# Optimization experiments

Hardware: AMD Instinct MI355X
Metric: run time of the kernel (lower is better)

Reference implementation:

```python
import jax, jax.numpy as jnp
import numpy as np

FRAME, LATENT, HIDDEN, GATE_H, EXPERTS = 267, 32, 256, 64, 6
BATCH = 4096
IN0 = LATENT + FRAME            # 299: decoder layer-0 input (z, c)
IN1 = LATENT + HIDDEN           # 288: decoder layer-1/2 input (z, h)
OUT = FRAME                     # num_future_predictions * frame_size


def _lin(key, fan_in, fan_out):
    b = np.sqrt(1.0 / fan_in)
    return jax.random.uniform(key, (fan_in, fan_out), jnp.float32, -b, b)


def setup_inputs() -> dict:
    key = jax.random.key(0)
    ks = jax.random.split(key, 16)
    d = {
        "x": jax.random.normal(ks[0], (BATCH, FRAME), jnp.float32),
        "c": jax.random.normal(ks[1], (BATCH, FRAME), jnp.float32),
        "eps": jax.random.normal(ks[2], (BATCH, LATENT), jnp.float32),
        # encoder
        "enc_w1": _lin(ks[3], 2 * FRAME, HIDDEN), "enc_b1": jnp.zeros((HIDDEN,), jnp.float32),
        "enc_w2": _lin(ks[4], FRAME + HIDDEN, HIDDEN), "enc_b2": jnp.zeros((HIDDEN,), jnp.float32),
        "enc_wmu": _lin(ks[5], FRAME + HIDDEN, LATENT), "enc_bmu": jnp.zeros((LATENT,), jnp.float32),
        "enc_wlv": _lin(ks[6], FRAME + HIDDEN, LATENT), "enc_blv": jnp.zeros((LATENT,), jnp.float32),
        # gate MLP
        "g_w0": _lin(ks[7], IN0, GATE_H), "g_b0": jnp.zeros((GATE_H,), jnp.float32),
        "g_w1": _lin(ks[8], GATE_H, GATE_H), "g_b1": jnp.zeros((GATE_H,), jnp.float32),
        "g_w2": _lin(ks[9], GATE_H, EXPERTS), "g_b2": jnp.zeros((EXPERTS,), jnp.float32),
        # expert-mixed decoder layers (kaiming-uniform-ish init, bias 0.01)
        "w0": jax.random.uniform(ks[10], (EXPERTS, IN0, HIDDEN), jnp.float32, -np.sqrt(6.0 / IN0), np.sqrt(6.0 / IN0)),
        "b0": jnp.full((EXPERTS, HIDDEN), 0.01, jnp.float32),
        "w1": jax.random.uniform(ks[11], (EXPERTS, IN1, HIDDEN), jnp.float32, -np.sqrt(6.0 / IN1), np.sqrt(6.0 / IN1)),
        "b1": jnp.full((EXPERTS, HIDDEN), 0.01, jnp.float32),
        "w2": jax.random.uniform(ks[12], (EXPERTS, IN1, OUT), jnp.float32, -np.sqrt(6.0 / IN1), np.sqrt(6.0 / IN1)),
        "b2": jnp.full((EXPERTS, OUT), 0.01, jnp.float32),
    }
    return d


def reference(x, c, eps,
              enc_w1, enc_b1, enc_w2, enc_b2, enc_wmu, enc_bmu, enc_wlv, enc_blv,
              g_w0, g_b0, g_w1, g_b1, g_w2, g_b2,
              w0, b0, w1, b1, w2, b2):
    elu = jax.nn.elu
    # --- encoder ---
    h1 = elu(jnp.concatenate([x, c], axis=1) @ enc_w1 + enc_b1)
    h2 = elu(jnp.concatenate([x, h1], axis=1) @ enc_w2 + enc_b2)
    s = jnp.concatenate([x, h2], axis=1)
    mu = s @ enc_wmu + enc_bmu
    logvar = s @ enc_wlv + enc_blv
    z = mu + eps * jnp.exp(0.5 * logvar)
    # --- gate ---
    zc = jnp.concatenate([z, c], axis=1)
    g = elu(zc @ g_w0 + g_b0)
    g = elu(g @ g_w1 + g_b1)
    coeff = jax.nn.softmax(g @ g_w2 + g_b2, axis=1)  # [N, E]
    # --- soft-MoE decoder: blended-weight per-sample GEMMs ---
    layer = c
    for w, b, act in ((w0, b0, elu), (w1, b1, elu), (w2, b2, None)):
        inp = jnp.concatenate([z, layer], axis=1)  # [N, Din]
        # out[n,o] = sum_e coeff[n,e] * (inp[n,:] @ w[e,:,o]) + coeff[n,:] @ b[:,o]
        out = jnp.einsum('ne,ni,eio->no', coeff, inp, w) + coeff @ b
        layer = act(out) if act is not None else out
    return layer, mu, logvar
```

## Files before the change

### kernel.cpp

```cpp
#include <hip/hip_runtime.h>
#include <hip/hip_bf16.h>
#include <math.h>

#define N_BATCH 4096
#define FRAME   267
#define LATENT  32
#define HIDDEN  256
#define GATE_H  64
#define EXPERTS 6

typedef __hip_bfloat16 bf16;
typedef __bf16  bf16x8 __attribute__((ext_vector_type(8)));
typedef float   f32x4  __attribute__((ext_vector_type(4)));

__device__ __forceinline__ float eluf(float v) { return (v > 0.f) ? v : (expf(v) - 1.f); }

#define MFMA(a, b, p) __builtin_amdgcn_mfma_f32_16x16x32_bf16((a), (b), (p), 0, 0, 0)

struct WEnt { const float* src; bf16* dst; int K, M, Mtot, mOff, Ksteps, Mtiles, cum; };
struct WTab { WEnt e[10]; int total; };

__global__ __launch_bounds__(256) void prep_kernel(
    const float* __restrict__ bmu, const float* __restrict__ blv,
    float* __restrict__ biasCat, WTab tab)
{
    const int tid = threadIdx.x, bid = blockIdx.x;
    if (bid == 0 && tid < 64)
        biasCat[tid] = (tid < 32) ? bmu[tid] : blv[tid - 32];

    __shared__ float tbuf[32][33];
    int i = 0;
    while (i < 9 && bid >= tab.e[i + 1].cum) ++i;
    const WEnt en = tab.e[i];
    const int t = bid - en.cum;
    const int perE = en.Ksteps * en.Mtiles;
    const int e = t / perE;
    const int rr = t - e * perE;
    const int mt = rr / en.Ksteps;
    const int ks = rr - mt * en.Ksteps;
    const int tx = tid & 31, ty = tid >> 5;
    const float* src = en.src + (size_t)e * en.K * en.M;
    #pragma unroll
    for (int i0 = 0; i0 < 32; i0 += 8) {
        const int k = ks * 32 + i0 + ty, m = mt * 32 + tx;
        tbuf[i0 + ty][tx] = (k < en.K && m < en.M) ? src[(size_t)k * en.M + m] : 0.f;
    }
    __syncthreads();
    bf16* dst = en.dst + ((size_t)(e * en.Ksteps + ks) * en.Mtot + en.mOff + mt * 32) * 32;
    #pragma unroll
    for (int i0 = 0; i0 < 32; i0 += 8)
        dst[(size_t)(i0 + ty) * 32 + tx] = __float2bfloat16(tbuf[tx][i0 + ty]);
}

__global__ __launch_bounds__(512, 2) void fused_kernel(
    const float* __restrict__ x, const float* __restrict__ c,
    const float* __restrict__ eps,
    const bf16* __restrict__ We1, const float* __restrict__ eb1,
    const bf16* __restrict__ We2, const float* __restrict__ eb2,
    const bf16* __restrict__ Wml, const float* __restrict__ biasCat,
    const bf16* __restrict__ Wg0, const float* __restrict__ gb0,
    const bf16* __restrict__ Wg1, const float* __restrict__ gb1,
    const bf16* __restrict__ Wg2, const float* __restrict__ gb2,
    const bf16* __restrict__ W0, const float* __restrict__ b0,
    const bf16* __restrict__ W1, const float* __restrict__ b1,
    const bf16* __restrict__ W2, const float* __restrict__ b2,
    float* __restrict__ out_layer, float* __restrict__ out_mu,
    float* __restrict__ out_lv)
{
    __shared__ bf16  bufA[16 * 552];
    __shared__ bf16  bufB[16 * 552];
    __shared__ float sML[16 * 64];
    __shared__ bf16  sG1[16 * 72];
    __shared__ bf16  sG2[16 * 72];
    __shared__ float sLg[16 * 16];
    __shared__ float sCo[EXPERTS * 16];

    const int tid  = threadIdx.x;
    const int w    = tid >> 6, lane = tid & 63, ml = lane & 15, quad = lane >> 4;
    const int row0 = blockIdx.x * 16;
    const int r32  = tid >> 5, l32 = tid & 31;

    {
        const float* xr = x + (size_t)(row0 + r32) * FRAME;
        const float* cr = c + (size_t)(row0 + r32) * FRAME;
        #pragma unroll
        for (int j = 0; j < 17; ++j) {
            const int col = l32 + j * 32;
            float v = 0.f;
            if (col < FRAME)          v = xr[col];
            else if (col < 2 * FRAME) v = cr[col - FRAME];
            bufA[r32 * 552 + col] = __float2bfloat16(v);
        }
    }
    __syncthreads();

    {
        bf16x8 av[17];
        #pragma unroll
        for (int ks = 0; ks < 17; ++ks)
            av[ks] = *(const bf16x8*)(bufA + ml * 552 + ks * 32 + quad * 8);
        const int col0 = 32 * w + ml;
        f32x4 p0 = (f32x4){0,0,0,0}, p1 = (f32x4){0,0,0,0};
        const bf16* wp = We1 + (size_t)col0 * 32 + quad * 8;
        #pragma unroll
        for (int ks = 0; ks < 17; ++ks) {
            p0 = MFMA(av[ks], *(const bf16x8*)(wp + (size_t)ks * 256 * 32), p0);
            p1 = MFMA(av[ks], *(const bf16x8*)(wp + (size_t)ks * 256 * 32 + 16 * 32), p1);
        }
        const float bv0 = eb1[col0], bv1 = eb1[col0 + 16];
        #pragma unroll
        for (int rg = 0; rg < 4; ++rg) {
            bufB[(quad * 4 + rg) * 552 + 267 + col0]      = __float2bfloat16(eluf(p0[rg] + bv0));
            bufB[(quad * 4 + rg) * 552 + 267 + col0 + 16] = __float2bfloat16(eluf(p1[rg] + bv1));
        }
        #pragma unroll
        for (int j = 0; j < 9; ++j) {
            const int cc = l32 + j * 32;
            if (cc < 267) bufB[r32 * 552 + cc] = bufA[r32 * 552 + cc];
            else          bufB[r32 * 552 + (cc - 267 + 523)] = __float2bfloat16(0.f);
        }
    }
    __syncthreads();

    {
        bf16x8 av[17];
        #pragma unroll
        for (int ks = 0; ks < 17; ++ks)
            av[ks] = *(const bf16x8*)(bufB + ml * 552 + ks * 32 + quad * 8);
        const int col0 = 32 * w + ml;
        f32x4 p0 = (f32x4){0,0,0,0}, p1 = (f32x4){0,0,0,0};
        const bf16* wp = We2 + (size_t)col0 * 32 + quad * 8;
        #pragma unroll
        for (int ks = 0; ks < 17; ++ks) {
            p0 = MFMA(av[ks], *(const bf16x8*)(wp + (size_t)ks * 256 * 32), p0);
            p1 = MFMA(av[ks], *(const bf16x8*)(wp + (size_t)ks * 256 * 32 + 16 * 32), p1);
        }
        __syncthreads();
        const float bv0 = eb2[col0], bv1 = eb2[col0 + 16];
        #pragma unroll
        for (int rg = 0; rg < 4; ++rg) {
            bufB[(quad * 4 + rg) * 552 + 267 + col0]      = __float2bfloat16(eluf(p0[rg] + bv0));
            bufB[(quad * 4 + rg) * 552 + 267 + col0 + 16] = __float2bfloat16(eluf(p1[rg] + bv1));
        }
    }
    __syncthreads();

    if (w < 4) {
        const int col = 16 * w + ml;
        f32x4 p = (f32x4){0,0,0,0};
        const bf16* wp = Wml + (size_t)col * 32 + quad * 8;
        #pragma unroll
        for (int ks = 0; ks < 17; ++ks) {
            const bf16x8 av = *(const bf16x8*)(bufB + ml * 552 + ks * 32 + quad * 8);
            p = MFMA(av, *(const bf16x8*)(wp + (size_t)ks * 64 * 32), p);
        }
        const float bv = biasCat[col];
        #pragma unroll
        for (int rg = 0; rg < 4; ++rg)
            sML[(quad * 4 + rg) * 64 + col] = p[rg] + bv;
    }
    __syncthreads();

    {
        const float m  = sML[r32 * 64 + l32];
        const float lv = sML[r32 * 64 + 32 + l32];
        const int gi = (row0 + r32) * LATENT + l32;
        out_mu[gi] = m; out_lv[gi] = lv;
        const bf16 zb = __float2bfloat16(m + eps[gi] * expf(0.5f * lv));
        bufA[r32 * 552 + l32] = zb;
        bufB[r32 * 552 + l32] = zb;
        #pragma unroll
        for (int j = 0; j < 9; ++j) {
            const int col = 32 + l32 + j * 32;
            bf16 v = __float2bfloat16(0.f);
            if (col < 299) v = bufA[r32 * 552 + 267 + (col - 32)];
            bufB[r32 * 552 + col] = v;
        }
    }
    __syncthreads();

    if (w < 4) {
        const int col = 16 * w + ml;
        f32x4 p = (f32x4){0,0,0,0};
        const bf16* wp = Wg0 + (size_t)col * 32 + quad * 8;
        #pragma unroll
        for (int ks = 0; ks < 10; ++ks)
            p = MFMA(*(const bf16x8*)(bufB + ml * 552 + ks * 32 + quad * 8),
                     *(const bf16x8*)(wp + (size_t)ks * 64 * 32), p);
        const float bv = gb0[col];
        #pragma unroll
        for (int rg = 0; rg < 4; ++rg)
            sG1[(quad * 4 + rg) * 72 + col] = __float2bfloat16(eluf(p[rg] + bv));
    }
    __syncthreads();

    if (w < 4) {
        const int col = 16 * w + ml;
        f32x4 p = (f32x4){0,0,0,0};
        const bf16* wp = Wg1 + (size_t)col * 32 + quad * 8;
        #pragma unroll
        for (int ks = 0; ks < 2; ++ks)
            p = MFMA(*(const bf16x8*)(sG1 + ml * 72 + ks * 32 + quad * 8),
                     *(const bf16x8*)(wp + (size_t)ks * 64 * 32), p);
        const float bv = gb1[col];
        #pragma unroll
        for (int rg = 0; rg < 4; ++rg)
            sG2[(quad * 4 + rg) * 72 + col] = __float2bfloat16(eluf(p[rg] + bv));
    }
    __syncthreads();

    if (w == 0) {
        f32x4 p = (f32x4){0,0,0,0};
        const bf16* wp = Wg2 + (size_t)ml * 32 + quad * 8;
        #pragma unroll
        for (int ks = 0; ks < 2; ++ks)
            p = MFMA(*(const bf16x8*)(sG2 + ml * 72 + ks * 32 + quad * 8),
                     *(const bf16x8*)(wp + (size_t)ks * 32 * 32), p);
        const float bv = (ml < EXPERTS) ? gb2[ml] : 0.f;
        #pragma unroll
        for (int rg = 0; rg < 4; ++rg)
            sLg[(quad * 4 + rg) * 16 + ml] = p[rg] + bv;
    }
    __syncthreads();

    if (tid < 16) {
        float v[EXPERTS];
        float m = -1e30f;
        #pragma unroll
        for (int i = 0; i < EXPERTS; ++i) { v[i] = sLg[tid * 16 + i]; m = fmaxf(m, v[i]); }
        float s = 0.f;
        #pragma unroll
        for (int i = 0; i < EXPERTS; ++i) { v[i] = expf(v[i] - m); s += v[i]; }
        const float inv = 1.f / s;
        #pragma unroll
        for (int i = 0; i < EXPERTS; ++i) sCo[i * 16 + tid] = v[i] * inv;
    }
    __syncthreads();

    {
        bf16x8 av[10];
        #pragma unroll
        for (int ks = 0; ks < 10; ++ks)
            av[ks] = *(const bf16x8*)(bufB + ml * 552 + ks * 32 + quad * 8);
        const int col0 = 32 * w + ml;
        f32x4 acc0 = (f32x4){0,0,0,0}, acc1 = (f32x4){0,0,0,0};
        for (int e = 0; e < EXPERTS; ++e) {
            f32x4 p0 = (f32x4){0,0,0,0}, p1 = (f32x4){0,0,0,0};
            const bf16* wp = W0 + ((size_t)e * 10 * 256 + col0) * 32 + quad * 8;
            #pragma unroll
            for (int ks = 0; ks < 10; ++ks) {
                p0 = MFMA(av[ks], *(const bf16x8*)(wp + (size_t)ks * 256 * 32), p0);
                p1 = MFMA(av[ks], *(const bf16x8*)(wp + (size_t)ks * 256 * 32 + 16 * 32), p1);
            }
            const float bv0 = b0[e * 256 + col0], bv1 = b0[e * 256 + col0 + 16];
            #pragma unroll
            for (int rg = 0; rg < 4; ++rg) {
                const float cf = sCo[e * 16 + quad * 4 + rg];
                acc0[rg] += cf * (p0[rg] + bv0);
                acc1[rg] += cf * (p1[rg] + bv1);
            }
        }
        #pragma unroll
        for (int rg = 0; rg < 4; ++rg) {
            bufA[(quad * 4 + rg) * 552 + 32 + col0]      = __float2bfloat16(eluf(acc0[rg]));
            bufA[(quad * 4 + rg) * 552 + 32 + col0 + 16] = __float2bfloat16(eluf(acc1[rg]));
        }
    }
    __syncthreads();

    {
        bf16x8 av[9];
        #pragma unroll
        for (int ks = 0; ks < 9; ++ks)
            av[ks] = *(const bf16x8*)(bufA + ml * 552 + ks * 32 + quad * 8);
        const int col0 = 32 * w + ml;
        f32x4 acc0 = (f32x4){0,0,0,0}, acc1 = (f32x4){0,0,0,0};
        for (int e = 0; e < EXPERTS; ++e) {
            f32x4 p0 = (f32x4){0,0,0,0}, p1 = (f32x4){0,0,0,0};
            const bf16* wp = W1 + ((size_t)e * 9 * 256 + col0) * 32 + quad * 8;
            #pragma unroll
            for (int ks = 0; ks < 9; ++ks) {
                p0 = MFMA(av[ks], *(const bf16x8*)(wp + (size_t)ks * 256 * 32), p0);
                p1 = MFMA(av[ks], *(const bf16x8*)(wp + (size_t)ks * 256 * 32 + 16 * 32), p1);
            }
            const float bv0 = b1[e * 256 + col0], bv1 = b1[e * 256 + col0 + 16];
            #pragma unroll
            for (int rg = 0; rg < 4; ++rg) {
                const float cf = sCo[e * 16 + quad * 4 + rg];
                acc0[rg] += cf * (p0[rg] + bv0);
                acc1[rg] += cf * (p1[rg] + bv1);
            }
        }
        __syncthreads();
        #pragma unroll
        for (int rg = 0; rg < 4; ++rg) {
            bufB[(quad * 4 + rg) * 552 + 32 + col0]      = __float2bfloat16(eluf(acc0[rg]));
            bufB[(quad * 4 + rg) * 552 + 32 + col0 + 16] = __float2bfloat16(eluf(acc1[rg]));
        }
    }
    __syncthreads();

    {
        bf16x8 av[9];
        #pragma unroll
        for (int ks = 0; ks < 9; ++ks)
            av[ks] = *(const bf16x8*)(bufB + ml * 552 + ks * 32 + quad * 8);
        for (int t = w; t < 18; t += 8) {
            const int col = 16 * t + ml;
            f32x4 acc = (f32x4){0,0,0,0};
            for (int e = 0; e < EXPERTS; ++e) {
                f32x4 p = (f32x4){0,0,0,0};
                const bf16* wp = W2 + ((size_t)e * 9 * 320 + col) * 32 + quad * 8;
                #pragma unroll
                for (int ks = 0; ks < 9; ++ks)
                    p = MFMA(av[ks], *(const bf16x8*)(wp + (size_t)ks * 320 * 32), p);
                const float bv = (col < FRAME) ? b2[e * FRAME + col] : 0.f;
                #pragma unroll
                for (int rg = 0; rg < 4; ++rg)
                    acc[rg] += sCo[e * 16 + quad * 4 + rg] * (p[rg] + bv);
            }
            if (col < FRAME) {
                #pragma unroll
                for (int rg = 0; rg < 4; ++rg)
                    out_layer[(size_t)(row0 + quad * 4 + rg) * FRAME + col] = acc[rg];
            }
        }
    }
}

extern "C" void kernel_launch(void* const* d_in, const int* in_sizes, int n_in,
                              void* d_out, int out_size, void* d_ws, size_t ws_size,
                              hipStream_t stream) {
    const float* x       = (const float*)d_in[0];
    const float* c       = (const float*)d_in[1];
    const float* eps     = (const float*)d_in[2];
    const float* enc_w1  = (const float*)d_in[3];
    const float* enc_b1  = (const float*)d_in[4];
    const float* enc_w2  = (const float*)d_in[5];
    const float* enc_b2  = (const float*)d_in[6];
    const float* enc_wmu = (const float*)d_in[7];
    const float* enc_bmu = (const float*)d_in[8];
    const float* enc_wlv = (const float*)d_in[9];
    const float* enc_blv = (const float*)d_in[10];
    const float* g_w0    = (const float*)d_in[11];
    const float* g_b0    = (const float*)d_in[12];
    const float* g_w1    = (const float*)d_in[13];
    const float* g_b1    = (const float*)d_in[14];
    const float* g_w2    = (const float*)d_in[15];
    const float* g_b2    = (const float*)d_in[16];
    const float* w0      = (const float*)d_in[17];
    const float* b0      = (const float*)d_in[18];
    const float* w1      = (const float*)d_in[19];
    const float* b1      = (const float*)d_in[20];
    const float* w2      = (const float*)d_in[21];
    const float* b2      = (const float*)d_in[22];

    float* out_layer = (float*)d_out;
    float* out_mu    = out_layer + (size_t)N_BATCH * FRAME;
    float* out_lv    = out_mu    + (size_t)N_BATCH * LATENT;

    char* p = (char*)d_ws;
    float* biasCat = (float*)p;  p += 64 * 4;
    bf16* Wt_e1 = (bf16*)p;      p += (size_t)17 * 256 * 32 * 2;
    bf16* Wt_e2 = (bf16*)p;      p += (size_t)17 * 256 * 32 * 2;
    bf16* Wt_ml = (bf16*)p;      p += (size_t)17 * 64 * 32 * 2;
    bf16* Wt_g0 = (bf16*)p;      p += (size_t)10 * 64 * 32 * 2;
    bf16* Wt_g1 = (bf16*)p;      p += (size_t)2 * 64 * 32 * 2;
    bf16* Wt_g2 = (bf16*)p;      p += (size_t)2 * 32 * 32 * 2;
    bf16* Wt_w0 = (bf16*)p;      p += (size_t)EXPERTS * 10 * 256 * 32 * 2;
    bf16* Wt_w1 = (bf16*)p;      p += (size_t)EXPERTS * 9 * 256 * 32 * 2;
    bf16* Wt_w2 = (bf16*)p;      p += (size_t)EXPERTS * 9 * 320 * 32 * 2;

    WTab tab;
    int cum = 0, n = 0;
    auto add = [&](const float* src, bf16* dst, int K, int M, int Mtot, int mOff, int E) {
        int Ksteps;
        if (K == 534 || K == 523) Ksteps = 17;
        else if (K == 299) Ksteps = 10;
        else if (K == 288) Ksteps = 9;
        else Ksteps = 2;
        const int Mtiles = (M + 31) / 32;
        tab.e[n] = {src, dst, K, M, Mtot, mOff, Ksteps, Mtiles, cum};
        cum += E * Ksteps * Mtiles;
        ++n;
    };
    add(enc_w1,  Wt_e1, 534, 256, 256, 0, 1);
    add(enc_w2,  Wt_e2, 523, 256, 256, 0, 1);
    add(enc_wmu, Wt_ml, 523, 32, 64, 0, 1);
    add(enc_wlv, Wt_ml, 523, 32, 64, 32, 1);
    add(g_w0,    Wt_g0, 299, 64, 64, 0, 1);
    add(g_w1,    Wt_g1, 64, 64, 64, 0, 1);
    add(g_w2,    Wt_g2, 64, 6, 32, 0, 1);
    add(w0,      Wt_w0, 299, 256, 256, 0, EXPERTS);
    add(w1,      Wt_w1, 288, 256, 256, 0, EXPERTS);
    add(w2,      Wt_w2, 288, 267, 320, 0, EXPERTS);
    tab.total = cum;

    prep_kernel<<<dim3(cum), dim3(256), 0, stream>>>(enc_bmu, enc_blv, biasCat, tab);

    fused_kernel<<<dim3(N_BATCH / 16), dim3(512), 0, stream>>>(
        x, c, eps,
        Wt_e1, enc_b1, Wt_e2, enc_b2, Wt_ml, biasCat,
        Wt_g0, g_b0, Wt_g1, g_b1, Wt_g2, g_b2,
        Wt_w0, b0, Wt_w1, b1, Wt_w2, b2,
        out_layer, out_mu, out_lv);
}
```

Before: 187.5 us.

## Double block to 1024 threads and overlap gate MLP with decoder layer-0 experts

The fused kernel now launches 16 waves per block instead of 8, with each wave computing one 16-column tile instead of two in the encoder and decoder GEMMs. Decoder layer 0 computes each expert's partial product into separate registers while the gate MLP and softmax run, and blends with the coefficients only after they are ready. This is meant to hide the serial gate chain behind MFMA work and raise wave-level parallelism. The cost is more registers per thread (six accumulators plus cached A fragments) and a tighter register budget under launch_bounds(1024,2), which could force spills. In the final layer 2 GEMM only 18 tiles exist for 16 waves, so two waves do a second tile and the load is uneven.

```diff
diff --git a/kernel.cpp b/kernel.cpp
--- a/kernel.cpp
+++ b/kernel.cpp
@@ -52,7 +52,7 @@
         dst[(size_t)(i0 + ty) * 32 + tx] = __float2bfloat16(tbuf[tx][i0 + ty]);
 }
 
-__global__ __launch_bounds__(512, 2) void fused_kernel(
+__global__ __launch_bounds__(1024, 2) void fused_kernel(
     const float* __restrict__ x, const float* __restrict__ c,
     const float* __restrict__ eps,
     const bf16* __restrict__ We1, const float* __restrict__ eb1,
@@ -78,70 +78,59 @@
     const int tid  = threadIdx.x;
     const int w    = tid >> 6, lane = tid & 63, ml = lane & 15, quad = lane >> 4;
     const int row0 = blockIdx.x * 16;
-    const int r32  = tid >> 5, l32 = tid & 31;
-
-    {
-        const float* xr = x + (size_t)(row0 + r32) * FRAME;
-        const float* cr = c + (size_t)(row0 + r32) * FRAME;
-        #pragma unroll
-        for (int j = 0; j < 17; ++j) {
-            const int col = l32 + j * 32;
-            float v = 0.f;
-            if (col < FRAME)          v = xr[col];
-            else if (col < 2 * FRAME) v = cr[col - FRAME];
-            bufA[r32 * 552 + col] = __float2bfloat16(v);
-        }
-    }
-    __syncthreads();
-
-    {
-        bf16x8 av[17];
-        #pragma unroll
-        for (int ks = 0; ks < 17; ++ks)
-            av[ks] = *(const bf16x8*)(bufA + ml * 552 + ks * 32 + quad * 8);
-        const int col0 = 32 * w + ml;
-        f32x4 p0 = (f32x4){0,0,0,0}, p1 = (f32x4){0,0,0,0};
-        const bf16* wp = We1 + (size_t)col0 * 32 + quad * 8;
+
+    {
+        const float* xr = x + (size_t)(row0 + w) * FRAME;
+        const float* cr = c + (size_t)(row0 + w) * FRAME;
+        #pragma unroll
+        for (int j = 0; j < 9; ++j) {
+            const int col = lane + j * 64;
+            if (col < 544) {
+                float v = 0.f;
+                if (col < FRAME)          v = xr[col];
+                else if (col < 2 * FRAME) v = cr[col - FRAME];
+                bufA[w * 552 + col] = __float2bfloat16(v);
+            }
+        }
+    }
+    __syncthreads();
+
+    {
+        const int col = 16 * w + ml;
+        f32x4 p = (f32x4){0,0,0,0};
+        const bf16* wp = We1 + (size_t)col * 32 + quad * 8;
         #pragma unroll
         for (int ks = 0; ks < 17; ++ks) {
-            p0 = MFMA(av[ks], *(const bf16x8*)(wp + (size_t)ks * 256 * 32), p0);
-            p1 = MFMA(av[ks], *(const bf16x8*)(wp + (size_t)ks * 256 * 32 + 16 * 32), p1);
-        }
-        const float bv0 = eb1[col0], bv1 = eb1[col0 + 16];
-        #pragma unroll
-        for (int rg = 0; rg < 4; ++rg) {
-            bufB[(quad * 4 + rg) * 552 + 267 + col0]      = __float2bfloat16(eluf(p0[rg] + bv0));
-            bufB[(quad * 4 + rg) * 552 + 267 + col0 + 16] = __float2bfloat16(eluf(p1[rg] + bv1));
-        }
-        #pragma unroll
-        for (int j = 0; j < 9; ++j) {
-            const int cc = l32 + j * 32;
-            if (cc < 267) bufB[r32 * 552 + cc] = bufA[r32 * 552 + cc];
-            else          bufB[r32 * 552 + (cc - 267 + 523)] = __float2bfloat16(0.f);
-        }
-    }
-    __syncthreads();
-
-    {
-        bf16x8 av[17];
-        #pragma unroll
-        for (int ks = 0; ks < 17; ++ks)
-            av[ks] = *(const bf16x8*)(bufB + ml * 552 + ks * 32 + quad * 8);
-        const int col0 = 32 * w + ml;
-        f32x4 p0 = (f32x4){0,0,0,0}, p1 = (f32x4){0,0,0,0};
-        const bf16* wp = We2 + (size_t)col0 * 32 + quad * 8;
+            const bf16x8 a = *(const bf16x8*)(bufA + ml * 552 + ks * 32 + quad * 8);
+            p = MFMA(a, *(const bf16x8*)(wp + (size_t)ks * 256 * 32), p);
+        }
+        const float bv = eb1[col];
+        #pragma unroll
+        for (int rg = 0; rg < 4; ++rg)
+            bufB[(quad * 4 + rg) * 552 + 267 + col] = __float2bfloat16(eluf(p[rg] + bv));
+        #pragma unroll
+        for (int j = 0; j < 5; ++j) {
+            const int cc = lane + j * 64;
+            if (cc < 267) bufB[w * 552 + cc] = bufA[w * 552 + cc];
+        }
+        if (lane < 21) bufB[w * 552 + 523 + lane] = __float2bfloat16(0.f);
+    }
+    __syncthreads();
+
+    {
+        const int col = 16 * w + ml;
+        f32x4 p = (f32x4){0,0,0,0};
+        const bf16* wp = We2 + (size_t)col * 32 + quad * 8;
         #pragma unroll
         for (int ks = 0; ks < 17; ++ks) {
-            p0 = MFMA(av[ks], *(const bf16x8*)(wp + (size_t)ks * 256 * 32), p0);
-            p1 = MFMA(av[ks], *(const bf16x8*)(wp + (size_t)ks * 256 * 32 + 16 * 32), p1);
-        }
-        __syncthreads();
-        const float bv0 = eb2[col0], bv1 = eb2[col0 + 16];
-        #pragma unroll
-        for (int rg = 0; rg < 4; ++rg) {
-            bufB[(quad * 4 + rg) * 552 + 267 + col0]      = __float2bfloat16(eluf(p0[rg] + bv0));
-            bufB[(quad * 4 + rg) * 552 + 267 + col0 + 16] = __float2bfloat16(eluf(p1[rg] + bv1));
-        }
+            const bf16x8 a = *(const bf16x8*)(bufB + ml * 552 + ks * 32 + quad * 8);
+            p = MFMA(a, *(const bf16x8*)(wp + (size_t)ks * 256 * 32), p);
+        }
+        __syncthreads();
+        const float bv = eb2[col];
+        #pragma unroll
+        for (int rg = 0; rg < 4; ++rg)
+            bufB[(quad * 4 + rg) * 552 + 267 + col] = __float2bfloat16(eluf(p[rg] + bv));
     }
     __syncthreads();
 
@@ -151,8 +140,8 @@
         const bf16* wp = Wml + (size_t)col * 32 + quad * 8;
         #pragma unroll
         for (int ks = 0; ks < 17; ++ks) {
-            const bf16x8 av = *(const bf16x8*)(bufB + ml * 552 + ks * 32 + quad * 8);
-            p = MFMA(av, *(const bf16x8*)(wp + (size_t)ks * 64 * 32), p);
+            const bf16x8 a = *(const bf16x8*)(bufB + ml * 552 + ks * 32 + quad * 8);
+            p = MFMA(a, *(const bf16x8*)(wp + (size_t)ks * 64 * 32), p);
         }
         const float bv = biasCat[col];
         #pragma unroll
@@ -161,142 +150,138 @@
     }
     __syncthreads();
 
-    {
-        const float m  = sML[r32 * 64 + l32];
-        const float lv = sML[r32 * 64 + 32 + l32];
-        const int gi = (row0 + r32) * LATENT + l32;
+    if (tid < 512) {
+        const int r = tid >> 5, l = tid & 31;
+        const float m  = sML[r * 64 + l];
+        const float lv = sML[r * 64 + 32 + l];
+        const int gi = (row0 + r) * LATENT + l;
         out_mu[gi] = m; out_lv[gi] = lv;
         const bf16 zb = __float2bfloat16(m + eps[gi] * expf(0.5f * lv));
-        bufA[r32 * 552 + l32] = zb;
-        bufB[r32 * 552 + l32] = zb;
+        bufA[r * 552 + l] = zb;
+        bufB[r * 552 + l] = zb;
         #pragma unroll
         for (int j = 0; j < 9; ++j) {
-            const int col = 32 + l32 + j * 32;
+            const int col = 32 + l + j * 32;
             bf16 v = __float2bfloat16(0.f);
-            if (col < 299) v = bufA[r32 * 552 + 267 + (col - 32)];
-            bufB[r32 * 552 + col] = v;
-        }
-    }
-    __syncthreads();
-
-    if (w < 4) {
-        const int col = 16 * w + ml;
-        f32x4 p = (f32x4){0,0,0,0};
-        const bf16* wp = Wg0 + (size_t)col * 32 + quad * 8;
-        #pragma unroll
-        for (int ks = 0; ks < 10; ++ks)
-            p = MFMA(*(const bf16x8*)(bufB + ml * 552 + ks * 32 + quad * 8),
-                     *(const bf16x8*)(wp + (size_t)ks * 64 * 32), p);
-        const float bv = gb0[col];
-        #pragma unroll
-        for (int rg = 0; rg < 4; ++rg)
-            sG1[(quad * 4 + rg) * 72 + col] = __float2bfloat16(eluf(p[rg] + bv));
-    }
-    __syncthreads();
-
-    if (w < 4) {
-        const int col = 16 * w + ml;
-        f32x4 p = (f32x4){0,0,0,0};
-        const bf16* wp = Wg1 + (size_t)col * 32 + quad * 8;
-        #pragma unroll
-        for (int ks = 0; ks < 2; ++ks)
-            p = MFMA(*(const bf16x8*)(sG1 + ml * 72 + ks * 32 + quad * 8),
-                     *(const bf16x8*)(wp + (size_t)ks * 64 * 32), p);
-        const float bv = gb1[col];
-        #pragma unroll
-        for (int rg = 0; rg < 4; ++rg)
-            sG2[(quad * 4 + rg) * 72 + col] = __float2bfloat16(eluf(p[rg] + bv));
-    }
-    __syncthreads();
-
-    if (w == 0) {
-        f32x4 p = (f32x4){0,0,0,0};
-        const bf16* wp = Wg2 + (size_t)ml * 32 + quad * 8;
-        #pragma unroll
-        for (int ks = 0; ks < 2; ++ks)
-            p = MFMA(*(const bf16x8*)(sG2 + ml * 72 + ks * 32 + quad * 8),
-                     *(const bf16x8*)(wp + (size_t)ks * 32 * 32), p);
-        const float bv = (ml < EXPERTS) ? gb2[ml] : 0.f;
-        #pragma unroll
-        for (int rg = 0; rg < 4; ++rg)
-            sLg[(quad * 4 + rg) * 16 + ml] = p[rg] + bv;
-    }
-    __syncthreads();
-
-    if (tid < 16) {
-        float v[EXPERTS];
-        float m = -1e30f;
-        #pragma unroll
-        for (int i = 0; i < EXPERTS; ++i) { v[i] = sLg[tid * 16 + i]; m = fmaxf(m, v[i]); }
-        float s = 0.f;
-        #pragma unroll
-        for (int i = 0; i < EXPERTS; ++i) { v[i] = expf(v[i] - m); s += v[i]; }
-        const float inv = 1.f / s;
-        #pragma unroll
-        for (int i = 0; i < EXPERTS; ++i) sCo[i * 16 + tid] = v[i] * inv;
-    }
-    __syncthreads();
-
-    {
+            if (col < 299) v = bufA[r * 552 + 267 + (col - 32)];
+            bufB[r * 552 + col] = v;
+        }
+    }
+    __syncthreads();
+
+    {
+        const int col = 16 * w + ml;
         bf16x8 av[10];
         #pragma unroll
         for (int ks = 0; ks < 10; ++ks)
             av[ks] = *(const bf16x8*)(bufB + ml * 552 + ks * 32 + quad * 8);
-        const int col0 = 32 * w + ml;
-        f32x4 acc0 = (f32x4){0,0,0,0}, acc1 = (f32x4){0,0,0,0};
-        for (int e = 0; e < EXPERTS; ++e) {
-            f32x4 p0 = (f32x4){0,0,0,0}, p1 = (f32x4){0,0,0,0};
-            const bf16* wp = W0 + ((size_t)e * 10 * 256 + col0) * 32 + quad * 8;
-            #pragma unroll
-            for (int ks = 0; ks < 10; ++ks) {
-                p0 = MFMA(av[ks], *(const bf16x8*)(wp + (size_t)ks * 256 * 32), p0);
-                p1 = MFMA(av[ks], *(const bf16x8*)(wp + (size_t)ks * 256 * 32 + 16 * 32), p1);
-            }
-            const float bv0 = b0[e * 256 + col0], bv1 = b0[e * 256 + col0 + 16];
-            #pragma unroll
-            for (int rg = 0; rg < 4; ++rg) {
-                const float cf = sCo[e * 16 + quad * 4 + rg];
-                acc0[rg] += cf * (p0[rg] + bv0);
-                acc1[rg] += cf * (p1[rg] + bv1);
-            }
-        }
-        #pragma unroll
-        for (int rg = 0; rg < 4; ++rg) {
-            bufA[(quad * 4 + rg) * 552 + 32 + col0]      = __float2bfloat16(eluf(acc0[rg]));
-            bufA[(quad * 4 + rg) * 552 + 32 + col0 + 16] = __float2bfloat16(eluf(acc1[rg]));
-        }
-    }
-    __syncthreads();
-
-    {
+
+        auto moe_part = [&](int e, f32x4& p) {
+            const bf16* wp = W0 + ((size_t)e * 10 * 256 + col) * 32 + quad * 8;
+            #pragma unroll
+            for (int ks = 0; ks < 10; ++ks)
+                p = MFMA(av[ks], *(const bf16x8*)(wp + (size_t)ks * 256 * 32), p);
+        };
+
+        f32x4 pe0 = (f32x4){0,0,0,0}, pe1 = (f32x4){0,0,0,0}, pe2 = (f32x4){0,0,0,0};
+        f32x4 pe3 = (f32x4){0,0,0,0}, pe4 = (f32x4){0,0,0,0}, pe5 = (f32x4){0,0,0,0};
+
+        if (w < 4) {
+            f32x4 p = (f32x4){0,0,0,0};
+            const bf16* wp = Wg0 + (size_t)col * 32 + quad * 8;
+            #pragma unroll
+            for (int ks = 0; ks < 10; ++ks)
+                p = MFMA(av[ks], *(const bf16x8*)(wp + (size_t)ks * 64 * 32), p);
+            const float bv = gb0[col];
+            #pragma unroll
+            for (int rg = 0; rg < 4; ++rg)
+                sG1[(quad * 4 + rg) * 72 + col] = __float2bfloat16(eluf(p[rg] + bv));
+        }
+        moe_part(0, pe0); moe_part(1, pe1);
+        __syncthreads();
+
+        if (w < 4) {
+            f32x4 p = (f32x4){0,0,0,0};
+            const bf16* wp = Wg1 + (size_t)col * 32 + quad * 8;
+            #pragma unroll
+            for (int ks = 0; ks < 2; ++ks)
+                p = MFMA(*(const bf16x8*)(sG1 + ml * 72 + ks * 32 + quad * 8),
+                         *(const bf16x8*)(wp + (size_t)ks * 64 * 32), p);
+            const float bv = gb1[col];
+            #pragma unroll
+            for (int rg = 0; rg < 4; ++rg)
+                sG2[(quad * 4 + rg) * 72 + col] = __float2bfloat16(eluf(p[rg] + bv));
+        }
+        moe_part(2, pe2); moe_part(3, pe3);
+        __syncthreads();
+
+        if (w == 0) {
+            f32x4 p = (f32x4){0,0,0,0};
+            const bf16* wp = Wg2 + (size_t)ml * 32 + quad * 8;
+            #pragma unroll
+            for (int ks = 0; ks < 2; ++ks)
+                p = MFMA(*(const bf16x8*)(sG2 + ml * 72 + ks * 32 + quad * 8),
+                         *(const bf16x8*)(wp + (size_t)ks * 32 * 32), p);
+            const float bv = (ml < EXPERTS) ? gb2[ml] : 0.f;
+            #pragma unroll
+            for (int rg = 0; rg < 4; ++rg)
+                sLg[(quad * 4 + rg) * 16 + ml] = p[rg] + bv;
+        }
+        moe_part(4, pe4);
+        __syncthreads();
+
+        if (tid < 16) {
+            float v[EXPERTS];
+            float m = -1e30f;
+            #pragma unroll
+            for (int i = 0; i < EXPERTS; ++i) { v[i] = sLg[tid * 16 + i]; m = fmaxf(m, v[i]); }
+            float s = 0.f;
+            #pragma unroll
+            for (int i = 0; i < EXPERTS; ++i) { v[i] = expf(v[i] - m); s += v[i]; }
+            const float inv = 1.f / s;
+            #pragma unroll
+            for (int i = 0; i < EXPERTS; ++i) sCo[i * 16 + tid] = v[i] * inv;
+        }
+        moe_part(5, pe5);
+        __syncthreads();
+
+        f32x4 acc = (f32x4){0,0,0,0};
+        auto blend = [&](const f32x4& p, int e) {
+            const float bv = b0[e * 256 + col];
+            #pragma unroll
+            for (int rg = 0; rg < 4; ++rg)
+                acc[rg] += sCo[e * 16 + quad * 4 + rg] * (p[rg] + bv);
+        };
+        blend(pe0, 0); blend(pe1, 1); blend(pe2, 2);
+        blend(pe3, 3); blend(pe4, 4); blend(pe5, 5);
+        #pragma unroll
+        for (int rg = 0; rg < 4; ++rg)
+            bufA[(quad * 4 + rg) * 552 + 32 + col] = __float2bfloat16(eluf(acc[rg]));
+    }
+    __syncthreads();
+
+    {
+        const int col = 16 * w + ml;
         bf16x8 av[9];
         #pragma unroll
         for (int ks = 0; ks < 9; ++ks)
             av[ks] = *(const bf16x8*)(bufA + ml * 552 + ks * 32 + quad * 8);
-        const int col0 = 32 * w + ml;
-        f32x4 acc0 = (f32x4){0,0,0,0}, acc1 = (f32x4){0,0,0,0};
+        f32x4 acc = (f32x4){0,0,0,0};
+        #pragma unroll
         for (int e = 0; e < EXPERTS; ++e) {
-            f32x4 p0 = (f32x4){0,0,0,0}, p1 = (f32x4){0,0,0,0};
-            const bf16* wp = W1 + ((size_t)e * 9 * 256 + col0) * 32 + quad * 8;
-            #pragma unroll
-            for (int ks = 0; ks < 9; ++ks) {
-                p0 = MFMA(av[ks], *(const bf16x8*)(wp + (size_t)ks * 256 * 32), p0);
-                p1 = MFMA(av[ks], *(const bf16x8*)(wp + (size_t)ks * 256 * 32 + 16 * 32), p1);
-            }
-            const float bv0 = b1[e * 256 + col0], bv1 = b1[e * 256 + col0 + 16];
-            #pragma unroll
-            for (int rg = 0; rg < 4; ++rg) {
-                const float cf = sCo[e * 16 + quad * 4 + rg];
-                acc0[rg] += cf * (p0[rg] + bv0);
-                acc1[rg] += cf * (p1[rg] + bv1);
-            }
-        }
-        __syncthreads();
-        #pragma unroll
-        for (int rg = 0; rg < 4; ++rg) {
-            bufB[(quad * 4 + rg) * 552 + 32 + col0]      = __float2bfloat16(eluf(acc0[rg]));
-            bufB[(quad * 4 + rg) * 552 + 32 + col0 + 16] = __float2bfloat16(eluf(acc1[rg]));
-        }
+            f32x4 p = (f32x4){0,0,0,0};
+            const bf16* wp = W1 + ((size_t)e * 9 * 256 + col) * 32 + quad * 8;
+            #pragma unroll
+            for (int ks = 0; ks < 9; ++ks)
+                p = MFMA(av[ks], *(const bf16x8*)(wp + (size_t)ks * 256 * 32), p);
+            const float bv = b1[e * 256 + col];
+            #pragma unroll
+            for (int rg = 0; rg < 4; ++rg)
+                acc[rg] += sCo[e * 16 + quad * 4 + rg] * (p[rg] + bv);
+        }
+        #pragma unroll
+        for (int rg = 0; rg < 4; ++rg)
+            bufB[(quad * 4 + rg) * 552 + 32 + col] = __float2bfloat16(eluf(acc[rg]));
     }
     __syncthreads();
 
@@ -305,9 +290,10 @@
         #pragma unroll
         for (int ks = 0; ks < 9; ++ks)
             av[ks] = *(const bf16x8*)(bufB + ml * 552 + ks * 32 + quad * 8);
-        for (int t = w; t < 18; t += 8) {
+        for (int t = w; t < 18; t += 16) {
             const int col = 16 * t + ml;
             f32x4 acc = (f32x4){0,0,0,0};
+            #pragma unroll
             for (int e = 0; e < EXPERTS; ++e) {
                 f32x4 p = (f32x4){0,0,0,0};
                 const bf16* wp = W2 + ((size_t)e * 9 * 320 + col) * 32 + quad * 8;
@@ -398,7 +384,7 @@
 
     prep_kernel<<<dim3(cum), dim3(256), 0, stream>>>(enc_bmu, enc_blv, biasCat, tab);
 
-    fused_kernel<<<dim3(N_BATCH / 16), dim3(512), 0, stream>>>(
+    fused_kernel<<<dim3(N_BATCH / 16), dim3(1024), 0, stream>>>(
         x, c, eps,
         Wt_e1, enc_b1, Wt_e2, enc_b2, Wt_ml, biasCat,
         Wt_g0, g_b0, Wt_g1, g_b1, Wt_g2, g_b2,
```

After: 171.8 us. -8.4%, faster.
